# Kernel optimization log

Hardware: AMD Instinct MI355X
Metric: run time of the kernel (lower is better)

The kernel has to match this reference:

```python
import jax, jax.numpy as jnp
import numpy as np

N, D, E, TOP_K = 2048, 512, 16, 2
HID = 4 * D
EPS = 1e-10


def setup_inputs() -> dict:
    key = jax.random.key(0)
    ks = jax.random.split(key, 8)
    s = 0.02
    return {
        "x": jax.random.normal(ks[0], (N, D), dtype=jnp.float32),
        "w_norm": jnp.ones((D,), dtype=jnp.float32),
        "Wr": jax.random.normal(ks[1], (D, E), dtype=jnp.float32) * s,
        "br": jnp.zeros((E,), dtype=jnp.float32),
        "W1": jax.random.normal(ks[2], (E, D, HID), dtype=jnp.float32) * s,
        "b1": jnp.zeros((E, HID), dtype=jnp.float32),
        "W2": jax.random.normal(ks[3], (E, HID, D), dtype=jnp.float32) * s,
        "b2": jnp.zeros((E, D), dtype=jnp.float32),
    }


def reference(x, w_norm, Wr, br, W1, b1, W2, b2):
    res = x
    # RMSNorm over feature dim (dim=1 in the torch code for 2D input)
    rms = jnp.sqrt(jnp.mean(x * x, axis=1, keepdims=True) + EPS)
    xn = w_norm * (x / rms)
    # Router: top-k over expert logits, softmax over the k selected logits
    logits = xn @ Wr + br                      # [N, E]
    top_p, top_i = jax.lax.top_k(logits, TOP_K)  # [N, k]
    top_p = jax.nn.softmax(top_p, axis=-1)
    # Dense per-token expert weights [N, E] (top-k indices are distinct)
    weight = jnp.zeros((x.shape[0], E), dtype=x.dtype)
    weight = weight.at[jnp.arange(x.shape[0])[:, None], top_i].add(top_p)
    # All-expert FFN (dense reference for the routed dispatch)
    h = jnp.einsum("nd,edh->enh", xn, W1) + b1[:, None, :]   # [E, N, 4D]
    y = jnp.einsum("enh,ehd->end", jax.nn.silu(h), W2) + b2[:, None, :]  # [E, N, D]
    out = jnp.einsum("end,ne->nd", y, weight)
    return out + res
```

## Files before the change

kernel.cpp:

```cpp
#include <hip/hip_runtime.h>

#define N_TOK 2048
#define DIM   512
#define NEXP  16
#define HID   2048
#define NSLOT (N_TOK*2)

typedef __attribute__((ext_vector_type(8))) short short8;
typedef __attribute__((ext_vector_type(4))) float floatx4;

__device__ __forceinline__ ushort f2bf(float f) {
    union { float f; unsigned u; } c; c.f = f;
    unsigned u = c.u;
    unsigned r = (u + 0x7fffu + ((u >> 16) & 1u)) >> 16;
    return (ushort)r;
}
__device__ __forceinline__ float bf2f(ushort u) {
    union { unsigned u; float f; } c; c.u = ((unsigned)u) << 16;
    return c.f;
}

__device__ __forceinline__ void gl_lds16(const void* g, void* l) {
    __builtin_amdgcn_global_load_lds(
        (const __attribute__((address_space(1))) unsigned int*)g,
        (__attribute__((address_space(3))) unsigned int*)l, 16, 0, 0);
}

__global__ __launch_bounds__(256)
void router_fused(const float* __restrict__ x, const float* __restrict__ w_norm,
                  const float* __restrict__ Wr, const float* __restrict__ br,
                  ushort* __restrict__ xn, int2* __restrict__ rec_e,
                  float2* __restrict__ rec_w)
{
    __shared__ float xs[16][516];
    __shared__ float wrT[16][516];

    const int tid  = threadIdx.x;
    const int wave = tid >> 6, lane = tid & 63;
    const int tblk = blockIdx.x * 16;

#pragma unroll
    for (int k = 0; k < 32; k++) {
        const int idx = tid + k * 256;
        wrT[idx & 15][idx >> 4] = Wr[idx];
    }

    const float4* wnp = (const float4*)w_norm;
    const float4 wa = wnp[lane], wb = wnp[lane + 64];
#pragma unroll
    for (int i = 0; i < 4; i++) {
        const int tl = wave * 4 + i, t = tblk + tl;
        const float4* xp = (const float4*)(x + (size_t)t * DIM);
        const float4 a = xp[lane], b = xp[lane + 64];
        float ss = a.x*a.x + a.y*a.y + a.z*a.z + a.w*a.w
                 + b.x*b.x + b.y*b.y + b.z*b.z + b.w*b.w;
#pragma unroll
        for (int m = 32; m >= 1; m >>= 1) ss += __shfl_xor(ss, m, 64);
        const float rinv = 1.f / sqrtf(ss * (1.f / (float)DIM) + 1e-10f);
        float4 na, nb;
        na.x = a.x * wa.x * rinv; na.y = a.y * wa.y * rinv;
        na.z = a.z * wa.z * rinv; na.w = a.w * wa.w * rinv;
        nb.x = b.x * wb.x * rinv; nb.y = b.y * wb.y * rinv;
        nb.z = b.z * wb.z * rinv; nb.w = b.w * wb.w * rinv;
        *(float4*)&xs[tl][lane * 4]       = na;
        *(float4*)&xs[tl][256 + lane * 4] = nb;
        ushort4 ua, ub;
        ua.x = f2bf(na.x); ua.y = f2bf(na.y); ua.z = f2bf(na.z); ua.w = f2bf(na.w);
        ub.x = f2bf(nb.x); ub.y = f2bf(nb.y); ub.z = f2bf(nb.z); ub.w = f2bf(nb.w);
        ushort4* xo = (ushort4*)(xn + (size_t)t * DIM);
        xo[lane] = ua; xo[lane + 64] = ub;
    }
    __syncthreads();

    const int tl = tid >> 4, e = tid & 15;
    const int t = tblk + tl;
    float acc = 0.f;
#pragma unroll 4
    for (int d = 0; d < DIM; d += 4) {
        const float4 xv = *(const float4*)&xs[tl][d];
        const float4 wv = *(const float4*)&wrT[e][d];
        acc += xv.x * wv.x + xv.y * wv.y + xv.z * wv.z + xv.w * wv.w;
    }
    const float v = acc + br[e];

    float m0 = v; int i0 = e; float m1 = -1e30f; int i1 = 16;
#pragma unroll
    for (int msk = 1; msk < 16; msk <<= 1) {
        const float om0 = __shfl_xor(m0, msk, 64); const int oi0 = __shfl_xor(i0, msk, 64);
        const float om1 = __shfl_xor(m1, msk, 64); const int oi1 = __shfl_xor(i1, msk, 64);
        const bool bf_ = (om0 > m0) || (om0 == m0 && oi0 < i0);
        const float t0m = bf_ ? om0 : m0; const int t0i = bf_ ? oi0 : i0;
        const float l0m = bf_ ? m0 : om0; const int l0i = bf_ ? i0 : oi0;
        const bool b2_ = (om1 > m1) || (om1 == m1 && oi1 < i1);
        const float t2m = b2_ ? om1 : m1; const int t2i = b2_ ? oi1 : i1;
        const bool lw = (l0m > t2m) || (l0m == t2m && l0i < t2i);
        m0 = t0m; i0 = t0i;
        m1 = lw ? l0m : t2m; i1 = lw ? l0i : t2i;
    }
    if (e == 0) {
        const float ex = expf(m1 - m0);
        const float w0 = 1.f / (1.f + ex);
        rec_e[t] = make_int2(i0, i1);
        rec_w[t] = make_float2(w0, ex * w0);
    }
}

__global__ __launch_bounds__(1024)
void plan_kernel(const int2* __restrict__ rec_e, int* __restrict__ cnt,
                 int* __restrict__ off, int* __restrict__ tok_of_slot,
                 int* __restrict__ rec_slot)
{
    __shared__ int soff[17];
    const int e = threadIdx.x >> 6;
    const int lane = threadIdx.x & 63;

    int total = 0;
    for (int c = 0; c < N_TOK / 64; c++) {
        const int2 er = rec_e[c * 64 + lane];
        const bool hit = (er.x == e) || (er.y == e);
        total += __popcll(__ballot(hit));
    }
    if (lane == 0) soff[e + 1] = total;
    __syncthreads();
    if (threadIdx.x == 0) {
        soff[0] = 0;
        for (int q = 1; q <= 16; q++) soff[q] += soff[q - 1];
    }
    __syncthreads();
    int base = soff[e];
    if (lane == 0) { cnt[e] = soff[e + 1] - base; off[e] = base; }

    for (int c = 0; c < N_TOK / 64; c++) {
        const int t = c * 64 + lane;
        const int2 er = rec_e[t];
        const bool hit = (er.x == e) || (er.y == e);
        const unsigned long long b = __ballot(hit);
        if (hit) {
            const int slot = base + __popcll(b & ((1ull << lane) - 1ull));
            tok_of_slot[slot] = t;
            const int which = (er.y == e) ? 1 : 0;
            rec_slot[t * 2 + which] = slot;
        }
        base += __popcll(b);
    }
}

template<int MODE>
__global__ __launch_bounds__(256)
void gemm_f32b(const ushort* __restrict__ A, int a_stride,
               const float* __restrict__ W, int NnW, int Ktot,
               const float* __restrict__ bias,
               const int* __restrict__ cnt, const int* __restrict__ off,
               const int* __restrict__ tok_of_slot,
               ushort* __restrict__ hout, ushort* __restrict__ yout)
{
    const int flat = blockIdx.x + (blockIdx.y << 5);
    const int x = flat & 7;
    const int g = flat >> 3;
    int e, mt, nb, z;
    if (MODE == 0) {
        e  = x + ((g >> 7) << 3);
        const int r = g & 127;
        nb = r & 31; mt = r >> 5; z = 0;
    } else {
        const int G = ((g >> 5) << 3) + x;
        e = G >> 2; z = G & 3;
        const int idx = g & 31;
        mt = idx >> 3; nb = idx & 7;
    }

    const int count = cnt[e];
    if (mt * 128 >= count) return;
    const int base = off[e];
    const int rows = min(128, count - mt * 128);
    const int n0   = nb * 64;
    const int kbeg = (MODE == 0) ? 0 : (z * 512);
    ushort* yp = (MODE == 0) ? nullptr : (yout + (size_t)z * NSLOT * DIM);

    __shared__ __align__(16) ushort As[2][128 * 32];
    __shared__ __align__(16) float  Bf[2][32 * 64];
    __shared__ int toks[128];

    const int tid = threadIdx.x;
    if (tid < 128) {
        const int r = tid < rows ? tid : rows - 1;
        const int slot = base + mt * 128 + r;
        toks[tid] = (MODE == 0) ? tok_of_slot[slot] : slot;
    }
    __syncthreads();

    const int lane = tid & 63;
    const int wid  = tid >> 6;
    const int wm = wid >> 1, wn = wid & 1;
    const int fr = lane & 15, fg = lane >> 4;

    const int rl  = lane >> 2;
    const int sko = ((lane & 3) ^ ((lane >> 4) & 3)) * 8;

    const ushort* aptr[2];
#pragma unroll
    for (int j = 0; j < 2; j++) {
        const int s = wid * 2 + j;
        aptr[j] = A + (size_t)toks[s * 16 + rl] * a_stride + kbeg + sko;
    }
    const float* bptr[2];
#pragma unroll
    for (int j = 0; j < 2; j++) {
        const int s = wid * 2 + j;
        bptr[j] = W + ((size_t)e * Ktot + kbeg + s * 4 + (lane >> 4)) * NnW
                    + n0 + (lane & 15) * 4;
    }

    floatx4 acc[4][2];
#pragma unroll
    for (int mi = 0; mi < 4; mi++)
#pragma unroll
        for (int ni = 0; ni < 2; ni++)
#pragma unroll
            for (int r = 0; r < 4; r++) acc[mi][ni][r] = 0.f;

#define STAGE(pb, ktn)                                                             \
    do {                                                                           \
        const int ka = (ktn) * 32;                                                 \
        const size_t kb = (size_t)(ktn) * 32 * NnW;                                \
        _Pragma("unroll")                                                          \
        for (int j = 0; j < 2; j++)                                                \
            gl_lds16(aptr[j] + ka, (void*)(&As[pb][(wid * 2 + j) * 512]));         \
        _Pragma("unroll")                                                          \
        for (int j = 0; j < 2; j++)                                                \
            gl_lds16(bptr[j] + kb, (void*)(&Bf[pb][(wid * 2 + j) * 256]));         \
    } while (0)

    int cur = 0;
    STAGE(0, 0);

    const int cxor = (fr >> 2) & 3;
    const int bcol = wn * 32 + fr;
    for (int kt = 0; kt < 16; kt++) {
        if (kt < 15) {
            STAGE(cur ^ 1, kt + 1);
            asm volatile("s_waitcnt vmcnt(4)" ::: "memory");
        } else {
            asm volatile("s_waitcnt vmcnt(0)" ::: "memory");
        }
        __builtin_amdgcn_s_barrier();
        __builtin_amdgcn_sched_barrier(0);

        __builtin_amdgcn_s_setprio(1);
        {
            const int co = (fg ^ cxor) * 8;
            short8 af[4], bfr[2];
#pragma unroll
            for (int mi = 0; mi < 4; mi++)
                af[mi] = *(const short8*)&As[cur][(wm * 64 + mi * 16 + fr) * 32 + co];
#pragma unroll
            for (int ni = 0; ni < 2; ni++) {
#pragma unroll
                for (int j = 0; j < 8; j++) {
                    const float f = Bf[cur][(fg * 8 + j) * 64 + bcol + ni * 16];
                    bfr[ni][j] = (short)f2bf(f);
                }
            }
#pragma unroll
            for (int mi = 0; mi < 4; mi++)
#pragma unroll
                for (int ni = 0; ni < 2; ni++)
                    acc[mi][ni] = __builtin_amdgcn_mfma_f32_16x16x32_bf16(af[mi], bfr[ni], acc[mi][ni], 0, 0, 0);
        }
        __builtin_amdgcn_s_setprio(0);

        __builtin_amdgcn_sched_barrier(0);
        __builtin_amdgcn_s_barrier();
        cur ^= 1;
    }
#undef STAGE

#pragma unroll
    for (int ni = 0; ni < 2; ni++) {
        const int gn = n0 + wn * 32 + ni * 16 + fr;
        const float bv = (MODE == 0) ? bias[e * HID + gn] : 0.f;
#pragma unroll
        for (int mi = 0; mi < 4; mi++) {
#pragma unroll
            for (int r = 0; r < 4; r++) {
                const int lm = wm * 64 + mi * 16 + fg * 4 + r;
                if (lm < rows) {
                    const int slot = base + mt * 128 + lm;
                    float v = acc[mi][ni][r];
                    if (MODE == 0) {
                        v += bv;
                        v = v / (1.f + __expf(-v));
                        hout[(size_t)slot * HID + gn] = f2bf(v);
                    } else {
                        yp[(size_t)slot * DIM + gn] = f2bf(v);
                    }
                }
            }
        }
    }
}

__global__ __launch_bounds__(128)
void gather_kernel(const float* __restrict__ x, const ushort* __restrict__ ypart,
                   const float* __restrict__ b2,
                   const int2* __restrict__ rec_e, const float2* __restrict__ rec_w,
                   const int2* __restrict__ rec_slot, float* __restrict__ out)
{
    const int t = blockIdx.x;
    const int d4 = threadIdx.x * 4;
    const int2 ei = rec_e[t];
    const float2 w = rec_w[t];
    const int2 sl = rec_slot[t];
    const float4 xv  = *(const float4*)(x  + (size_t)t * DIM + d4);
    float4 s0 = make_float4(0.f, 0.f, 0.f, 0.f);
    float4 s1 = make_float4(0.f, 0.f, 0.f, 0.f);
#pragma unroll
    for (int kc = 0; kc < 4; kc++) {
        const ushort* yp = ypart + (size_t)kc * NSLOT * DIM;
        const ushort4 a = *(const ushort4*)(yp + (size_t)sl.x * DIM + d4);
        const ushort4 b = *(const ushort4*)(yp + (size_t)sl.y * DIM + d4);
        s0.x += bf2f(a.x); s0.y += bf2f(a.y); s0.z += bf2f(a.z); s0.w += bf2f(a.w);
        s1.x += bf2f(b.x); s1.y += bf2f(b.y); s1.z += bf2f(b.z); s1.w += bf2f(b.w);
    }
    const float4 b0  = *(const float4*)(b2 + (size_t)ei.x * DIM + d4);
    const float4 b1v = *(const float4*)(b2 + (size_t)ei.y * DIM + d4);
    float4 o;
    o.x = xv.x + w.x * (s0.x + b0.x) + w.y * (s1.x + b1v.x);
    o.y = xv.y + w.x * (s0.y + b0.y) + w.y * (s1.y + b1v.y);
    o.z = xv.z + w.x * (s0.z + b0.z) + w.y * (s1.z + b1v.z);
    o.w = xv.w + w.x * (s0.w + b0.w) + w.y * (s1.w + b1v.w);
    *(float4*)(out + (size_t)t * DIM + d4) = o;
}

extern "C" void kernel_launch(void* const* d_in, const int* in_sizes, int n_in,
                              void* d_out, int out_size, void* d_ws, size_t ws_size,
                              hipStream_t stream)
{
    const float* x  = (const float*)d_in[0];
    const float* wn = (const float*)d_in[1];
    const float* Wr = (const float*)d_in[2];
    const float* br = (const float*)d_in[3];
    const float* W1 = (const float*)d_in[4];
    const float* b1 = (const float*)d_in[5];
    const float* W2 = (const float*)d_in[6];
    const float* b2 = (const float*)d_in[7];
    float* out = (float*)d_out;

    char* ws = (char*)d_ws;
    ushort* xn    = (ushort*)(ws);
    ushort* h_buf = (ushort*)(ws + (2u  << 20));
    ushort* y_par = (ushort*)(ws + (18u << 20));
    char* p = ws + (40u << 20);
    int*    cnt         = (int*)p;    p += 256;
    int*    off         = (int*)p;    p += 256;
    int2*   rec_e       = (int2*)p;   p += N_TOK * 8;
    float2* rec_w       = (float2*)p; p += N_TOK * 8;
    int2*   rec_slot    = (int2*)p;   p += N_TOK * 8;
    int*    tok_of_slot = (int*)p;    p += NSLOT * 4;

    router_fused<<<N_TOK / 16, 256, 0, stream>>>(x, wn, Wr, br, xn, rec_e, rec_w);

    plan_kernel<<<1, 1024, 0, stream>>>(rec_e, cnt, off, tok_of_slot, (int*)rec_slot);

    gemm_f32b<0><<<dim3(32, 64), 256, 0, stream>>>(
        xn, DIM, W1, HID, DIM, b1, cnt, off, tok_of_slot, h_buf, nullptr);

    gemm_f32b<1><<<dim3(32, 64), 256, 0, stream>>>(
        h_buf, HID, W2, DIM, HID, nullptr, cnt, off, nullptr, nullptr, y_par);

    gather_kernel<<<N_TOK, 128, 0, stream>>>(x, y_par, b2, rec_e, rec_w, rec_slot, out);
}
```

Before: 107.1 us.

## Enlarge expert GEMM tile to 256 rows and stage B as bf16 in LDS

Each block of the two routed expert GEMMs now covers 256 token rows instead of 128, with every wave owning 64 rows by the full 64 columns. Weights are loaded into registers, converted to bf16 once and written to LDS in a swizzled layout. This replaces per-wave fp32 LDS reads followed by conversion on every use, so each weight tile is reused across more rows and conversion work drops. In exchange the grid is doubled to cover the new index mapping, more blocks exit early for experts with few tokens, register pressure rises, and the register-staged B load adds a wait-and-write step in every k iteration.

```diff
diff --git a/kernel.cpp b/kernel.cpp
--- a/kernel.cpp
+++ b/kernel.cpp
@@ -159,133 +159,143 @@
     const int g = flat >> 3;
     int e, mt, nb, z;
     if (MODE == 0) {
-        e  = x + ((g >> 7) << 3);
-        const int r = g & 127;
+        e  = x + ((g >> 8) << 3);
+        const int r = g & 255;
         nb = r & 31; mt = r >> 5; z = 0;
     } else {
-        const int G = ((g >> 5) << 3) + x;
+        const int G = ((g >> 6) << 3) + x;
         e = G >> 2; z = G & 3;
-        const int idx = g & 31;
-        mt = idx >> 3; nb = idx & 7;
+        const int idx = g & 63;
+        nb = idx & 7; mt = idx >> 3;
     }
 
     const int count = cnt[e];
-    if (mt * 128 >= count) return;
+    if (mt * 256 >= count) return;
     const int base = off[e];
-    const int rows = min(128, count - mt * 128);
+    const int rows = min(256, count - mt * 256);
     const int n0   = nb * 64;
     const int kbeg = (MODE == 0) ? 0 : (z * 512);
     ushort* yp = (MODE == 0) ? nullptr : (yout + (size_t)z * NSLOT * DIM);
 
-    __shared__ __align__(16) ushort As[2][128 * 32];
-    __shared__ __align__(16) float  Bf[2][32 * 64];
-    __shared__ int toks[128];
+    __shared__ __align__(16) ushort As_[2 * 8192];
+    __shared__ __align__(16) ushort Bs_[2 * 2048];
+    __shared__ int toks[256];
 
     const int tid = threadIdx.x;
-    if (tid < 128) {
+    if (tid < 256) {
         const int r = tid < rows ? tid : rows - 1;
-        const int slot = base + mt * 128 + r;
+        const int slot = base + mt * 256 + r;
         toks[tid] = (MODE == 0) ? tok_of_slot[slot] : slot;
     }
     __syncthreads();
 
     const int lane = tid & 63;
     const int wid  = tid >> 6;
-    const int wm = wid >> 1, wn = wid & 1;
     const int fr = lane & 15, fg = lane >> 4;
 
     const int rl  = lane >> 2;
     const int sko = ((lane & 3) ^ ((lane >> 4) & 3)) * 8;
 
-    const ushort* aptr[2];
-#pragma unroll
-    for (int j = 0; j < 2; j++) {
-        const int s = wid * 2 + j;
+    const ushort* aptr[4];
+#pragma unroll
+    for (int j = 0; j < 4; j++) {
+        const int s = wid * 4 + j;
         aptr[j] = A + (size_t)toks[s * 16 + rl] * a_stride + kbeg + sko;
     }
-    const float* bptr[2];
-#pragma unroll
-    for (int j = 0; j < 2; j++) {
-        const int s = wid * 2 + j;
-        bptr[j] = W + ((size_t)e * Ktot + kbeg + s * 4 + (lane >> 4)) * NnW
-                    + n0 + (lane & 15) * 4;
-    }
-
-    floatx4 acc[4][2];
+    const float* bsrc = W + ((size_t)e * Ktot + kbeg + wid * 8) * NnW + n0 + lane;
+    const int bwoff = lane * 32 + ((wid ^ ((lane >> 1) & 3)) * 8);
+
+    float breg[8];
+#define LOADB(ktn)                                                           \
+    do {                                                                     \
+        _Pragma("unroll")                                                    \
+        for (int j = 0; j < 8; j++)                                          \
+            breg[j] = bsrc[((size_t)(ktn) * 32 + j) * NnW];                  \
+    } while (0)
+#define WRITEB(pb)                                                           \
+    do {                                                                     \
+        short8 bw;                                                           \
+        _Pragma("unroll")                                                    \
+        for (int j = 0; j < 8; j++) bw[j] = (short)f2bf(breg[j]);            \
+        *(short8*)&Bs_[(pb) * 2048 + bwoff] = bw;                            \
+    } while (0)
+#define STAGEA(pb, k0)                                                       \
+    do {                                                                     \
+        _Pragma("unroll")                                                    \
+        for (int j = 0; j < 4; j++)                                          \
+            gl_lds16(aptr[j] + (k0), (void*)(&As_[(pb) * 8192 + (wid * 4 + j) * 512])); \
+    } while (0)
+
+    floatx4 acc[4][4];
 #pragma unroll
     for (int mi = 0; mi < 4; mi++)
 #pragma unroll
-        for (int ni = 0; ni < 2; ni++)
+        for (int ni = 0; ni < 4; ni++)
 #pragma unroll
             for (int r = 0; r < 4; r++) acc[mi][ni][r] = 0.f;
 
-#define STAGE(pb, ktn)                                                             \
-    do {                                                                           \
-        const int ka = (ktn) * 32;                                                 \
-        const size_t kb = (size_t)(ktn) * 32 * NnW;                                \
-        _Pragma("unroll")                                                          \
-        for (int j = 0; j < 2; j++)                                                \
-            gl_lds16(aptr[j] + ka, (void*)(&As[pb][(wid * 2 + j) * 512]));         \
-        _Pragma("unroll")                                                          \
-        for (int j = 0; j < 2; j++)                                                \
-            gl_lds16(bptr[j] + kb, (void*)(&Bf[pb][(wid * 2 + j) * 256]));         \
-    } while (0)
+    STAGEA(0, 0);
+    LOADB(0);
+    asm volatile("s_waitcnt vmcnt(0)" ::: "memory");
+    WRITEB(0);
 
     int cur = 0;
-    STAGE(0, 0);
-
     const int cxor = (fr >> 2) & 3;
-    const int bcol = wn * 32 + fr;
+    const int cxb  = (fr >> 1) & 3;
     for (int kt = 0; kt < 16; kt++) {
         if (kt < 15) {
-            STAGE(cur ^ 1, kt + 1);
-            asm volatile("s_waitcnt vmcnt(4)" ::: "memory");
+            LOADB(kt + 1);
+            STAGEA(cur ^ 1, (kt + 1) * 32);
+            asm volatile("s_waitcnt vmcnt(12) lgkmcnt(0)" ::: "memory");
         } else {
-            asm volatile("s_waitcnt vmcnt(0)" ::: "memory");
+            asm volatile("s_waitcnt vmcnt(0) lgkmcnt(0)" ::: "memory");
         }
         __builtin_amdgcn_s_barrier();
         __builtin_amdgcn_sched_barrier(0);
 
         __builtin_amdgcn_s_setprio(1);
         {
-            const int co = (fg ^ cxor) * 8;
-            short8 af[4], bfr[2];
+            const int co  = (fg ^ cxor) * 8;
+            const int cob = (fg ^ cxb) * 8;
+            short8 af[4], bfr[4];
 #pragma unroll
             for (int mi = 0; mi < 4; mi++)
-                af[mi] = *(const short8*)&As[cur][(wm * 64 + mi * 16 + fr) * 32 + co];
-#pragma unroll
-            for (int ni = 0; ni < 2; ni++) {
-#pragma unroll
-                for (int j = 0; j < 8; j++) {
-                    const float f = Bf[cur][(fg * 8 + j) * 64 + bcol + ni * 16];
-                    bfr[ni][j] = (short)f2bf(f);
-                }
-            }
+                af[mi] = *(const short8*)&As_[cur * 8192 + (wid * 64 + mi * 16 + fr) * 32 + co];
+#pragma unroll
+            for (int ni = 0; ni < 4; ni++)
+                bfr[ni] = *(const short8*)&Bs_[cur * 2048 + (ni * 16 + fr) * 32 + cob];
 #pragma unroll
             for (int mi = 0; mi < 4; mi++)
 #pragma unroll
-                for (int ni = 0; ni < 2; ni++)
+                for (int ni = 0; ni < 4; ni++)
                     acc[mi][ni] = __builtin_amdgcn_mfma_f32_16x16x32_bf16(af[mi], bfr[ni], acc[mi][ni], 0, 0, 0);
         }
         __builtin_amdgcn_s_setprio(0);
 
         __builtin_amdgcn_sched_barrier(0);
         __builtin_amdgcn_s_barrier();
+
+        if (kt < 15) {
+            asm volatile("s_waitcnt vmcnt(4)" ::: "memory");
+            WRITEB(cur ^ 1);
+        }
         cur ^= 1;
     }
-#undef STAGE
-
-#pragma unroll
-    for (int ni = 0; ni < 2; ni++) {
-        const int gn = n0 + wn * 32 + ni * 16 + fr;
+#undef LOADB
+#undef WRITEB
+#undef STAGEA
+
+#pragma unroll
+    for (int ni = 0; ni < 4; ni++) {
+        const int gn = n0 + ni * 16 + fr;
         const float bv = (MODE == 0) ? bias[e * HID + gn] : 0.f;
 #pragma unroll
         for (int mi = 0; mi < 4; mi++) {
 #pragma unroll
             for (int r = 0; r < 4; r++) {
-                const int lm = wm * 64 + mi * 16 + fg * 4 + r;
+                const int lm = wid * 64 + mi * 16 + fg * 4 + r;
                 if (lm < rows) {
-                    const int slot = base + mt * 128 + lm;
+                    const int slot = base + mt * 256 + lm;
                     float v = acc[mi][ni][r];
                     if (MODE == 0) {
                         v += bv;
@@ -362,10 +372,10 @@
 
     plan_kernel<<<1, 1024, 0, stream>>>(rec_e, cnt, off, tok_of_slot, (int*)rec_slot);
 
-    gemm_f32b<0><<<dim3(32, 64), 256, 0, stream>>>(
+    gemm_f32b<0><<<dim3(32, 128), 256, 0, stream>>>(
         xn, DIM, W1, HID, DIM, b1, cnt, off, tok_of_slot, h_buf, nullptr);
 
-    gemm_f32b<1><<<dim3(32, 64), 256, 0, stream>>>(
+    gemm_f32b<1><<<dim3(32, 128), 256, 0, stream>>>(
         h_buf, HID, W2, DIM, HID, nullptr, cnt, off, nullptr, nullptr, y_par);
 
     gather_kernel<<<N_TOK, 128, 0, stream>>>(x, y_par, b2, rec_e, rec_w, rec_slot, out);
```

After: 108.1 us. Within noise of the previous version (+0.9%).
